# Optimization experiments

Hardware: AMD Instinct MI355X
Metric: run time of the kernel (lower is better)

The kernel has to match this reference:

```python
import jax, jax.numpy as jnp
import numpy as np

N = 20000       # num_nodes
B = 4           # batch
D = 32          # input_dim
OUT = 64        # output_dim
S = 2           # n_supports
E = 640000      # edges per support (avg degree 32)
MAX_STEP = 3
M = MAX_STEP * S + 1  # num_metrics = 7


def setup_inputs() -> dict:
    key = jax.random.key(0)
    k = jax.random.split(key, 6)
    inputs = jax.random.normal(k[0], (B, N, D), dtype=jnp.float32)
    edge_src = jax.random.randint(k[1], (S, E), 0, N, dtype=jnp.int32)
    edge_dst = jax.random.randint(k[2], (S, E), 0, N, dtype=jnp.int32)
    # ~1/deg scaled values so the diffusion recurrence stays numerically tame
    edge_vals = jax.random.uniform(k[3], (S, E), dtype=jnp.float32) / 32.0
    W = jax.random.normal(k[4], (OUT, D * M), dtype=jnp.float32) * 0.05
    bias = jnp.zeros((OUT,), dtype=jnp.float32)
    return dict(inputs=inputs, edge_vals=edge_vals, W=W, bias=bias,
                edge_src=edge_src, edge_dst=edge_dst)


def _spmm(vals, src, dst, x):
    # y[i] = sum_{edges (i<-j)} vals * x[j]  == support.mm(x) for COO support
    return jax.ops.segment_sum(vals[:, None] * x[src], dst, num_segments=N)


def reference(inputs, edge_vals, W, bias, edge_src, edge_dst):
    b, n, d = inputs.shape
    # x0: [N, D*B], batch fastest (matches permute([1,2,0]).reshape(n,-1))
    x0 = jnp.transpose(inputs, (1, 2, 0)).reshape(n, -1)
    xs = [x0]
    for s in range(S):
        v, sr, ds = edge_vals[s], edge_src[s], edge_dst[s]
        x1 = _spmm(v, sr, ds, x0)
        xs.append(x1)
        for _ in range(2, MAX_STEP + 1):
            x2 = 2.0 * _spmm(v, sr, ds, x1) - x0
            xs.append(x2)
            # NOTE: faithful to source aliasing quirk — x0 is mutated here,
            # so the next support starts from the mutated x0.
            x1, x0 = x2, x1
    x = jnp.stack(xs, 0)                       # [M, N, D*B]
    x = x.reshape(-1, n, d, b)                 # [M, N, D, B]
    x = jnp.transpose(x, (3, 1, 2, 0))         # [B, N, D, M]
    x = x.reshape(b, n, -1)                    # [B, N, D*M], M fastest
    return x @ W.T + bias                      # [B, N, OUT]
```

## Files before the change

kernel.cpp:

```cpp
#include <hip/hip_runtime.h>

#define N_NODES 20000
#define BATCH   4
#define DIN     32
#define DOUT    64
#define MSTEPS  7
#define ROW     128
#define NROW    896
#define NROWU   448
#define PLN     656
#define NT      79
#define KB2     (2 * NT)
#define CHUNK   2048
#define SLOT    12288
#define WSLOT   3584
#define RGRID   (N_NODES / 4)
#define PGRID   625
#define TGRID   10000

typedef short  short8 __attribute__((ext_vector_type(8)));
typedef float  f32x4  __attribute__((ext_vector_type(4)));

__device__ __forceinline__ unsigned short f2bf(float f) {
    unsigned u = __float_as_uint(f);
    unsigned r = u + 0x7fff + ((u >> 16) & 1);
    return (unsigned short)(r >> 16);
}
__device__ __forceinline__ float bf_lo(unsigned p) { return __uint_as_float(p << 16); }
__device__ __forceinline__ float bf_hi(unsigned p) { return __uint_as_float(p & 0xffff0000u); }

__global__ void init_k(int* __restrict__ cursor) {
    if (threadIdx.x < KB2) cursor[threadIdx.x] = threadIdx.x * SLOT;
}

__global__ void __launch_bounds__(256) p2t_k(const int* __restrict__ src,
                                             const int* __restrict__ dst,
                                             const float* __restrict__ vals,
                                             int* __restrict__ cursor,
                                             uint2* __restrict__ staged,
                                             const float* __restrict__ in,
                                             unsigned short* __restrict__ xs, int E) {
    __shared__ int lhist[KB2];
    __shared__ int lbase[KB2];
    __shared__ int gbase[KB2];
    __shared__ int sc[256];
    __shared__ uint2 buf[CHUNK];
    __shared__ unsigned short kk[CHUNK];
    int t = threadIdx.x;
    if (blockIdx.x >= PGRID) {
        int tid = (blockIdx.x - PGRID) * 256 + t;
        if (tid < N_NODES * ROW) {
            int b = tid & 3;
            int d = (tid >> 2) & 31;
            int n = tid >> 7;
            xs[(size_t)n * NROW + d * 4 + b] = f2bf(in[(b * N_NODES + n) * DIN + d]);
        }
        return;
    }
    int base = blockIdx.x * CHUNK;
    int nval = min(CHUNK, 2 * E - base);
    for (int i = t; i < KB2; i += 256) lhist[i] = 0;
    __syncthreads();
    int k[CHUNK / 256], pos[CHUNK / 256];
    uint2 pay[CHUNK / 256];
#pragma unroll
    for (int j = 0; j < CHUNK / 256; ++j) {
        int i = j * 256 + t;
        int e = base + i;
        if (i < nval) {
            int s = (e >= E) ? 1 : 0;
            int d = dst[e];
            pay[j] = make_uint2((unsigned)src[e] | ((unsigned)f2bf(vals[e]) << 16),
                                (unsigned)d);
            k[j] = s * NT + (d >> 8);
            pos[j] = atomicAdd(&lhist[k[j]], 1);
        } else k[j] = -1;
    }
    __syncthreads();
    int v = (t < KB2) ? lhist[t] : 0;
    sc[t] = v;
    __syncthreads();
    for (int off = 1; off < 256; off <<= 1) {
        int a = (t >= off) ? sc[t - off] : 0;
        __syncthreads();
        sc[t] += a;
        __syncthreads();
    }
    if (t < KB2) lbase[t] = sc[t] - v;
    __syncthreads();
    if (t < KB2 && lhist[t]) gbase[t] = atomicAdd(&cursor[t], lhist[t]);
#pragma unroll
    for (int j = 0; j < CHUNK / 256; ++j) {
        if (k[j] >= 0) {
            int slot = lbase[k[j]] + pos[j];
            buf[slot] = pay[j];
            kk[slot] = (unsigned short)k[j];
        }
    }
    __syncthreads();
#pragma unroll
    for (int j = 0; j < CHUNK / 256; ++j) {
        int i = j * 256 + t;
        if (i < nval) {
            int b = kk[i];
            staged[gbase[b] + (i - lbase[b])] = buf[i];
        }
    }
}

__global__ void __launch_bounds__(256) p3_fine_k(const uint2* __restrict__ staged,
                                                 const int* __restrict__ cursor,
                                                 int2* __restrict__ row_desc,
                                                 unsigned* __restrict__ csr) {
    __shared__ int lhist[64];
    __shared__ int sc[64];
    __shared__ int lcur[64];
    int bb = blockIdx.x;
    int b = bb >> 2, sub = bb & 3;
    int s = b / NT, tile = b - s * NT;
    int w0loc = sub * 64;
    int seg0 = b * SLOT;
    int len = cursor[b] - seg0;
    int t = threadIdx.x;
    if (t < 64) lhist[t] = 0;
    __syncthreads();
    for (int i = t; i < len; i += 256) {
        int dl = (int)(staged[seg0 + i].y & 255) - w0loc;
        if (dl >= 0 && dl < 64) atomicAdd(&lhist[dl], 1);
    }
    __syncthreads();
    int cntr = (t < 64) ? lhist[t] : 0;
    int pl = (cntr + 7) & ~7;
    if (t < 64) sc[t] = pl;
    __syncthreads();
    for (int off = 1; off < 64; off <<= 1) {
        int a = (t < 64 && t >= off) ? sc[t - off] : 0;
        __syncthreads();
        if (t < 64) sc[t] += a;
        __syncthreads();
    }
    int wbase = bb * WSLOT;
    if (t < 64) {
        int excl = sc[t] - pl;
        lcur[t] = wbase + excl;
        int nd = tile * 256 + w0loc + t;
        if (nd < N_NODES) row_desc[s * N_NODES + nd] = make_int2(wbase + excl, pl);
    }
    __syncthreads();
    for (int i = t; i < len; i += 256) {
        uint2 u = staged[seg0 + i];
        int dl = (int)(u.y & 255) - w0loc;
        if (dl >= 0 && dl < 64) {
            int p = atomicAdd(&lcur[dl], 1);
            csr[p] = u.x;
        }
    }
    if (t < 64) {
        int excl = sc[t] - pl;
        for (int i = cntr; i < pl; ++i) csr[wbase + excl + i] = 0u;
    }
}

__device__ __forceinline__ void spmm_core(const int2* __restrict__ rdesc,
                                          const unsigned* __restrict__ csr,
                                          const unsigned* __restrict__ xb,
                                          const unsigned* __restrict__ xprevb,
                                          unsigned* __restrict__ yb,
                                          float alpha, int node, int lane) {
    int2 rd = rdesc[node];
    int start = rd.x, end = rd.x + rd.y;
    float l0 = 0.f, h0 = 0.f, l1 = 0.f, h1 = 0.f;
    float l2 = 0.f, h2 = 0.f, l3 = 0.f, h3 = 0.f;
    for (int e = start; e < end; e += 8) {
        unsigned c0 = csr[e],     c1 = csr[e + 1], c2 = csr[e + 2], c3 = csr[e + 3];
        unsigned c4 = csr[e + 4], c5 = csr[e + 5], c6 = csr[e + 6], c7 = csr[e + 7];
        unsigned p0 = xb[(size_t)(c0 & 0xffffu) * NROWU + lane];
        unsigned p1 = xb[(size_t)(c1 & 0xffffu) * NROWU + lane];
        unsigned p2 = xb[(size_t)(c2 & 0xffffu) * NROWU + lane];
        unsigned p3 = xb[(size_t)(c3 & 0xffffu) * NROWU + lane];
        unsigned p4 = xb[(size_t)(c4 & 0xffffu) * NROWU + lane];
        unsigned p5 = xb[(size_t)(c5 & 0xffffu) * NROWU + lane];
        unsigned p6 = xb[(size_t)(c6 & 0xffffu) * NROWU + lane];
        unsigned p7 = xb[(size_t)(c7 & 0xffffu) * NROWU + lane];
        float v0 = bf_hi(c0), v1 = bf_hi(c1), v2 = bf_hi(c2), v3 = bf_hi(c3);
        float v4 = bf_hi(c4), v5 = bf_hi(c5), v6 = bf_hi(c6), v7 = bf_hi(c7);
        l0 = fmaf(v0, bf_lo(p0), l0);  h0 = fmaf(v0, bf_hi(p0), h0);
        l1 = fmaf(v1, bf_lo(p1), l1);  h1 = fmaf(v1, bf_hi(p1), h1);
        l2 = fmaf(v2, bf_lo(p2), l2);  h2 = fmaf(v2, bf_hi(p2), h2);
        l3 = fmaf(v3, bf_lo(p3), l3);  h3 = fmaf(v3, bf_hi(p3), h3);
        l0 = fmaf(v4, bf_lo(p4), l0);  h0 = fmaf(v4, bf_hi(p4), h0);
        l1 = fmaf(v5, bf_lo(p5), l1);  h1 = fmaf(v5, bf_hi(p5), h1);
        l2 = fmaf(v6, bf_lo(p6), l2);  h2 = fmaf(v6, bf_hi(p6), h2);
        l3 = fmaf(v7, bf_lo(p7), l3);  h3 = fmaf(v7, bf_hi(p7), h3);
    }
    float r0 = alpha * ((l0 + l1) + (l2 + l3));
    float r1 = alpha * ((h0 + h1) + (h2 + h3));
    if (xprevb) {
        unsigned pp = xprevb[(size_t)node * NROWU + lane];
        r0 -= bf_lo(pp);
        r1 -= bf_hi(pp);
    }
    yb[(size_t)node * NROWU + lane] = (unsigned)f2bf(r0) | ((unsigned)f2bf(r1) << 16);
}

__global__ void __launch_bounds__(256) spmm_row_k(const int2* __restrict__ rdesc,
                                                  const unsigned* __restrict__ csr,
                                                  const unsigned short* __restrict__ x,
                                                  const unsigned short* __restrict__ xprev,
                                                  unsigned short* __restrict__ y, float alpha) {
    int node = __builtin_amdgcn_readfirstlane(blockIdx.x * 4 + (threadIdx.x >> 6));
    int lane = threadIdx.x & 63;
    spmm_core(rdesc, csr, (const unsigned*)x, (const unsigned*)xprev, (unsigned*)y,
              alpha, node, lane);
}

__global__ void __launch_bounds__(256) spmm_dual_k(const int2* __restrict__ rdA,
                                                   const int2* __restrict__ rdB,
                                                   const unsigned* __restrict__ csr,
                                                   const unsigned short* __restrict__ x,
                                                   const unsigned short* __restrict__ xprevA,
                                                   unsigned short* __restrict__ yA,
                                                   unsigned short* __restrict__ yB) {
    int bid = blockIdx.x;
    int second = (bid >= RGRID) ? 1 : 0;
    int node = __builtin_amdgcn_readfirstlane((bid - second * RGRID) * 4 + (threadIdx.x >> 6));
    int lane = threadIdx.x & 63;
    const int2* rd = second ? rdB : rdA;
    const unsigned* xprevb = second ? nullptr : (const unsigned*)xprevA;
    unsigned* yb = second ? (unsigned*)yB : (unsigned*)yA;
    float alpha = second ? 1.0f : 2.0f;
    spmm_core(rd, csr, (const unsigned*)x, xprevb, yb, alpha, node, lane);
}

__global__ void __launch_bounds__(256) epilogue_mfma_k(const unsigned short* __restrict__ xs,
                                                       const float* __restrict__ W,
                                                       const float* __restrict__ bias,
                                                       float* __restrict__ out) {
    __shared__ unsigned short Alds[28 * PLN];
    int tid = threadIdx.x;
    int lane = tid & 63, ot = tid >> 6;
    int col = lane & 15, quad = lane >> 4;
    int o = ot * 16 + col;

    short8 bfrag[MSTEPS];
#pragma unroll
    for (int m = 0; m < MSTEPS; ++m) {
        short8 bf;
#pragma unroll
        for (int j = 0; j < 8; ++j)
            bf[j] = (short)f2bf(W[o * 224 + (quad * 8 + j) * 7 + m]);
        bfrag[m] = bf;
    }
    float bo = bias[o];

    int n0 = blockIdx.x * 16;
    const uint4* src = (const uint4*)(xs + (size_t)n0 * NROW);
#pragma unroll
    for (int it = 0; it < 7; ++it) {
        int idx = tid + it * 256;
        uint4 q = src[idx];
        int r    = idx / 112;
        int off8 = idx - r * 112;
        int m    = off8 >> 4;
        int d0   = (off8 & 15) * 2;
        unsigned vals[4] = {q.x, q.y, q.z, q.w};
#pragma unroll
        for (int h = 0; h < 4; ++h) {
            int dd = d0 + (h >> 1);
            int bA = (2 * h) & 3, bB = (2 * h + 1) & 3;
            Alds[(bA * 7 + m) * PLN + r * 40 + dd] = (unsigned short)(vals[h] & 0xffffu);
            Alds[(bB * 7 + m) * PLN + r * 40 + dd] = (unsigned short)(vals[h] >> 16);
        }
    }
    __syncthreads();

    f32x4 acc[BATCH];
#pragma unroll
    for (int b = 0; b < BATCH; ++b)
        acc[b] = (f32x4){bo, bo, bo, bo};

#pragma unroll
    for (int m = 0; m < MSTEPS; ++m) {
#pragma unroll
        for (int b = 0; b < BATCH; ++b) {
            short8 a = *(const short8*)&Alds[(b * 7 + m) * PLN + col * 40 + quad * 8];
            acc[b] = __builtin_amdgcn_mfma_f32_16x16x32_bf16(a, bfrag[m], acc[b], 0, 0, 0);
        }
    }

#pragma unroll
    for (int b = 0; b < BATCH; ++b) {
#pragma unroll
        for (int reg = 0; reg < 4; ++reg) {
            int n = n0 + quad * 4 + reg;
            out[((size_t)b * N_NODES + n) * DOUT + o] = acc[b][reg];
        }
    }
}

extern "C" void kernel_launch(void* const* d_in, const int* in_sizes, int n_in,
                              void* d_out, int out_size, void* d_ws, size_t ws_size,
                              hipStream_t stream) {
    const float* inputs    = (const float*)d_in[0];
    const float* edge_vals = (const float*)d_in[1];
    const float* W         = (const float*)d_in[2];
    const float* bias      = (const float*)d_in[3];
    const int*   edge_src  = (const int*)d_in[4];
    const int*   edge_dst  = (const int*)d_in[5];
    float* out = (float*)d_out;
    const int E = in_sizes[1] / 2;

    unsigned short* xs = (unsigned short*)d_ws;
    uint2* staged  = (uint2*)(xs + (size_t)N_NODES * NROW);
    unsigned* csr  = (unsigned*)(staged + (size_t)KB2 * SLOT);
    int* cursor    = (int*)(csr + (size_t)4 * KB2 * WSLOT);
    int2* row_desc = (int2*)(cursor + KB2 + 2);

    const int epgrid = N_NODES / 16;

    init_k<<<1, 256, 0, stream>>>(cursor);
    p2t_k<<<PGRID + TGRID, 256, 0, stream>>>(edge_src, edge_dst, edge_vals, cursor,
                                             staged, inputs, xs, E);
    p3_fine_k<<<4 * KB2, 256, 0, stream>>>(staged, cursor, row_desc, csr);

    const int2* rd0 = row_desc;
    const int2* rd1 = row_desc + N_NODES;

    unsigned short* X0 = xs + 0 * ROW;
    unsigned short* X1 = xs + 1 * ROW;
    unsigned short* X2 = xs + 2 * ROW;
    unsigned short* X3 = xs + 3 * ROW;
    unsigned short* X4 = xs + 4 * ROW;
    unsigned short* X5 = xs + 5 * ROW;
    unsigned short* X6 = xs + 6 * ROW;

    spmm_row_k<<<RGRID, 256, 0, stream>>>(rd0, csr, X0, nullptr, X1, 1.0f);
    spmm_row_k<<<RGRID, 256, 0, stream>>>(rd0, csr, X1, X0,      X2, 2.0f);
    spmm_dual_k<<<2 * RGRID, 256, 0, stream>>>(rd0, rd1, csr, X2, X1, X3, X4);
    spmm_row_k<<<RGRID, 256, 0, stream>>>(rd1, csr, X4, X2, X5, 2.0f);
    spmm_row_k<<<RGRID, 256, 0, stream>>>(rd1, csr, X5, X4, X6, 2.0f);

    epilogue_mfma_k<<<epgrid, 256, 0, stream>>>(xs, W, bias, out);
}
```

Baseline: 235.9 us.

## Fuse SpMM diffusion chain into one persistent kernel with grid barriers

Replaces the five separate SpMM launches with a single persistent kernel of 1024 blocks. Waves loop over nodes, and the dependent steps are separated by software grid-wide barriers built from an atomic counter. The aim is to remove launch gaps and per-launch ramp-up and tail costs between the dependent diffusion steps. In exchange it relies on all 1024 blocks being co-resident, since otherwise the barrier deadlocks. It also adds spin-wait cost and gives up the oversubscribed grid that helped hide latency.

```diff
diff --git a/kernel.cpp b/kernel.cpp
--- a/kernel.cpp
+++ b/kernel.cpp
@@ -14,9 +14,10 @@
 #define CHUNK   2048
 #define SLOT    12288
 #define WSLOT   3584
-#define RGRID   (N_NODES / 4)
 #define PGRID   625
 #define TGRID   10000
+#define CGRID   1024
+#define CWAVES  (CGRID * 4)
 
 typedef short  short8 __attribute__((ext_vector_type(8)));
 typedef float  f32x4  __attribute__((ext_vector_type(4)));
@@ -31,6 +32,7 @@
 
 __global__ void init_k(int* __restrict__ cursor) {
     if (threadIdx.x < KB2) cursor[threadIdx.x] = threadIdx.x * SLOT;
+    if (threadIdx.x == KB2) cursor[KB2] = 0;
 }
 
 __global__ void __launch_bounds__(256) p2t_k(const int* __restrict__ src,
@@ -203,33 +205,58 @@
     yb[(size_t)node * NROWU + lane] = (unsigned)f2bf(r0) | ((unsigned)f2bf(r1) << 16);
 }
 
-__global__ void __launch_bounds__(256) spmm_row_k(const int2* __restrict__ rdesc,
-                                                  const unsigned* __restrict__ csr,
-                                                  const unsigned short* __restrict__ x,
-                                                  const unsigned short* __restrict__ xprev,
-                                                  unsigned short* __restrict__ y, float alpha) {
-    int node = __builtin_amdgcn_readfirstlane(blockIdx.x * 4 + (threadIdx.x >> 6));
+__device__ __forceinline__ void gbar(int* bar, int phase) {
+    __syncthreads();
+    if (threadIdx.x == 0) {
+        __threadfence();
+        __hip_atomic_fetch_add(bar, 1, __ATOMIC_ACQ_REL, __HIP_MEMORY_SCOPE_AGENT);
+        int target = phase * CGRID;
+        while (__hip_atomic_load(bar, __ATOMIC_ACQUIRE, __HIP_MEMORY_SCOPE_AGENT) < target)
+            __builtin_amdgcn_s_sleep(2);
+        __threadfence();
+    }
+    __syncthreads();
+}
+
+__global__ void __launch_bounds__(256, 4) spmm_chain_k(const int2* __restrict__ rd0,
+                                                       const int2* __restrict__ rd1,
+                                                       const unsigned* __restrict__ csr,
+                                                       unsigned short* __restrict__ xs,
+                                                       int* __restrict__ bar) {
+    int wid = blockIdx.x * 4 + (threadIdx.x >> 6);
     int lane = threadIdx.x & 63;
-    spmm_core(rdesc, csr, (const unsigned*)x, (const unsigned*)xprev, (unsigned*)y,
-              alpha, node, lane);
-}
-
-__global__ void __launch_bounds__(256) spmm_dual_k(const int2* __restrict__ rdA,
-                                                   const int2* __restrict__ rdB,
-                                                   const unsigned* __restrict__ csr,
-                                                   const unsigned short* __restrict__ x,
-                                                   const unsigned short* __restrict__ xprevA,
-                                                   unsigned short* __restrict__ yA,
-                                                   unsigned short* __restrict__ yB) {
-    int bid = blockIdx.x;
-    int second = (bid >= RGRID) ? 1 : 0;
-    int node = __builtin_amdgcn_readfirstlane((bid - second * RGRID) * 4 + (threadIdx.x >> 6));
-    int lane = threadIdx.x & 63;
-    const int2* rd = second ? rdB : rdA;
-    const unsigned* xprevb = second ? nullptr : (const unsigned*)xprevA;
-    unsigned* yb = second ? (unsigned*)yB : (unsigned*)yA;
-    float alpha = second ? 1.0f : 2.0f;
-    spmm_core(rd, csr, (const unsigned*)x, xprevb, yb, alpha, node, lane);
+    unsigned* X0 = (unsigned*)xs + 0 * 64;
+    unsigned* X1 = (unsigned*)xs + 1 * 64;
+    unsigned* X2 = (unsigned*)xs + 2 * 64;
+    unsigned* X3 = (unsigned*)xs + 3 * 64;
+    unsigned* X4 = (unsigned*)xs + 4 * 64;
+    unsigned* X5 = (unsigned*)xs + 5 * 64;
+    unsigned* X6 = (unsigned*)xs + 6 * 64;
+
+    for (int n = wid; n < N_NODES; n += CWAVES)
+        spmm_core(rd0, csr, X0, nullptr, X1, 1.0f,
+                  __builtin_amdgcn_readfirstlane(n), lane);
+    gbar(bar, 1);
+    for (int n = wid; n < N_NODES; n += CWAVES)
+        spmm_core(rd0, csr, X1, X0, X2, 2.0f,
+                  __builtin_amdgcn_readfirstlane(n), lane);
+    gbar(bar, 2);
+    for (int t = wid; t < 2 * N_NODES; t += CWAVES) {
+        if (t < N_NODES)
+            spmm_core(rd0, csr, X2, X1, X3, 2.0f,
+                      __builtin_amdgcn_readfirstlane(t), lane);
+        else
+            spmm_core(rd1, csr, X2, nullptr, X4, 1.0f,
+                      __builtin_amdgcn_readfirstlane(t - N_NODES), lane);
+    }
+    gbar(bar, 3);
+    for (int n = wid; n < N_NODES; n += CWAVES)
+        spmm_core(rd1, csr, X4, X2, X5, 2.0f,
+                  __builtin_amdgcn_readfirstlane(n), lane);
+    gbar(bar, 4);
+    for (int n = wid; n < N_NODES; n += CWAVES)
+        spmm_core(rd1, csr, X5, X4, X6, 2.0f,
+                  __builtin_amdgcn_readfirstlane(n), lane);
 }
 
 __global__ void __launch_bounds__(256) epilogue_mfma_k(const unsigned short* __restrict__ xs,
@@ -315,6 +342,7 @@
     unsigned* csr  = (unsigned*)(staged + (size_t)KB2 * SLOT);
     int* cursor    = (int*)(csr + (size_t)4 * KB2 * WSLOT);
     int2* row_desc = (int2*)(cursor + KB2 + 2);
+    int* bar       = cursor + KB2;
 
     const int epgrid = N_NODES / 16;
 
@@ -326,19 +354,7 @@
     const int2* rd0 = row_desc;
     const int2* rd1 = row_desc + N_NODES;
 
-    unsigned short* X0 = xs + 0 * ROW;
-    unsigned short* X1 = xs + 1 * ROW;
-    unsigned short* X2 = xs + 2 * ROW;
-    unsigned short* X3 = xs + 3 * ROW;
-    unsigned short* X4 = xs + 4 * ROW;
-    unsigned short* X5 = xs + 5 * ROW;
-    unsigned short* X6 = xs + 6 * ROW;
-
-    spmm_row_k<<<RGRID, 256, 0, stream>>>(rd0, csr, X0, nullptr, X1, 1.0f);
-    spmm_row_k<<<RGRID, 256, 0, stream>>>(rd0, csr, X1, X0,      X2, 2.0f);
-    spmm_dual_k<<<2 * RGRID, 256, 0, stream>>>(rd0, rd1, csr, X2, X1, X3, X4);
-    spmm_row_k<<<RGRID, 256, 0, stream>>>(rd1, csr, X4, X2, X5, 2.0f);
-    spmm_row_k<<<RGRID, 256, 0, stream>>>(rd1, csr, X5, X4, X6, 2.0f);
+    spmm_chain_k<<<CGRID, 256, 0, stream>>>(rd0, rd1, csr, xs, bar);
 
     epilogue_mfma_k<<<epgrid, 256, 0, stream>>>(xs, W, bias, out);
 }
```

New measurement: 903.4 us. 283% more time.

## Build CSR via global histogram, scan, and atomic scatter instead of bucket staging

Applied to the files above, without the earlier changes.

Replaces the two-pass bucketed staging CSR build with a classic counting-sort pipeline: zero a per-row histogram, count degrees with global atomics, block-scan padded degrees, add block offsets and zero-pad, then scatter each edge directly into its CSR slot through per-row atomic cursors. This drops the intermediate staged buffer and its second read pass. In exchange it adds extra kernel launches and relies on global atomics with poor scatter locality. Row order within the CSR also becomes nondeterministic.

```diff
diff --git a/kernel.cpp b/kernel.cpp
--- a/kernel.cpp
+++ b/kernel.cpp
@@ -9,13 +9,9 @@
 #define NROW    896
 #define NROWU   448
 #define PLN     656
-#define NT      79
-#define KB2     (2 * NT)
-#define CHUNK   2048
-#define SLOT    12288
-#define WSLOT   3584
+#define NROWS2  (2 * N_NODES)
+#define SBLK    157
 #define RGRID   (N_NODES / 4)
-#define PGRID   625
 #define TGRID   10000
 
 typedef short  short8 __attribute__((ext_vector_type(8)));
@@ -29,56 +25,29 @@
 __device__ __forceinline__ float bf_lo(unsigned p) { return __uint_as_float(p << 16); }
 __device__ __forceinline__ float bf_hi(unsigned p) { return __uint_as_float(p & 0xffff0000u); }
 
-__global__ void init_k(int* __restrict__ cursor) {
-    if (threadIdx.x < KB2) cursor[threadIdx.x] = threadIdx.x * SLOT;
-}
-
-__global__ void __launch_bounds__(256) p2t_k(const int* __restrict__ src,
-                                             const int* __restrict__ dst,
-                                             const float* __restrict__ vals,
-                                             int* __restrict__ cursor,
-                                             uint2* __restrict__ staged,
-                                             const float* __restrict__ in,
-                                             unsigned short* __restrict__ xs, int E) {
-    __shared__ int lhist[KB2];
-    __shared__ int lbase[KB2];
-    __shared__ int gbase[KB2];
+__global__ void __launch_bounds__(256) zero_k(int* __restrict__ hist) {
+    int i = blockIdx.x * 256 + threadIdx.x;
+    if (i < NROWS2) hist[i] = 0;
+}
+
+__global__ void __launch_bounds__(256) hist_k(const int* __restrict__ dst,
+                                              int* __restrict__ hist, int E) {
+    int e = blockIdx.x * 256 + threadIdx.x;
+    if (e < 2 * E) {
+        int s = (e >= E) ? N_NODES : 0;
+        atomicAdd(&hist[s + dst[e]], 1);
+    }
+}
+
+__global__ void __launch_bounds__(256) scan1_k(const int* __restrict__ hist,
+                                               int2* __restrict__ row_desc,
+                                               int* __restrict__ bsum) {
     __shared__ int sc[256];
-    __shared__ uint2 buf[CHUNK];
-    __shared__ unsigned short kk[CHUNK];
     int t = threadIdx.x;
-    if (blockIdx.x >= PGRID) {
-        int tid = (blockIdx.x - PGRID) * 256 + t;
-        if (tid < N_NODES * ROW) {
-            int b = tid & 3;
-            int d = (tid >> 2) & 31;
-            int n = tid >> 7;
-            xs[(size_t)n * NROW + d * 4 + b] = f2bf(in[(b * N_NODES + n) * DIN + d]);
-        }
-        return;
-    }
-    int base = blockIdx.x * CHUNK;
-    int nval = min(CHUNK, 2 * E - base);
-    for (int i = t; i < KB2; i += 256) lhist[i] = 0;
-    __syncthreads();
-    int k[CHUNK / 256], pos[CHUNK / 256];
-    uint2 pay[CHUNK / 256];
-#pragma unroll
-    for (int j = 0; j < CHUNK / 256; ++j) {
-        int i = j * 256 + t;
-        int e = base + i;
-        if (i < nval) {
-            int s = (e >= E) ? 1 : 0;
-            int d = dst[e];
-            pay[j] = make_uint2((unsigned)src[e] | ((unsigned)f2bf(vals[e]) << 16),
-                                (unsigned)d);
-            k[j] = s * NT + (d >> 8);
-            pos[j] = atomicAdd(&lhist[k[j]], 1);
-        } else k[j] = -1;
-    }
-    __syncthreads();
-    int v = (t < KB2) ? lhist[t] : 0;
-    sc[t] = v;
+    int i = blockIdx.x * 256 + t;
+    int deg = (i < NROWS2) ? hist[i] : 0;
+    int pl = (deg + 7) & ~7;
+    sc[t] = pl;
     __syncthreads();
     for (int off = 1; off < 256; off <<= 1) {
         int a = (t >= off) ? sc[t - off] : 0;
@@ -86,78 +55,59 @@
         sc[t] += a;
         __syncthreads();
     }
-    if (t < KB2) lbase[t] = sc[t] - v;
+    if (i < NROWS2) row_desc[i] = make_int2(sc[t] - pl, pl);
+    if (t == 255) bsum[blockIdx.x] = sc[t];
+}
+
+__global__ void __launch_bounds__(256) fin_k(int2* __restrict__ row_desc,
+                                             const int* __restrict__ bsum,
+                                             const int* __restrict__ hist,
+                                             int* __restrict__ cursor,
+                                             unsigned* __restrict__ csr) {
+    __shared__ int red[256];
+    int t = threadIdx.x;
+    int blk = blockIdx.x;
+    red[t] = (t < blk) ? bsum[t] : 0;
     __syncthreads();
-    if (t < KB2 && lhist[t]) gbase[t] = atomicAdd(&cursor[t], lhist[t]);
-#pragma unroll
-    for (int j = 0; j < CHUNK / 256; ++j) {
-        if (k[j] >= 0) {
-            int slot = lbase[k[j]] + pos[j];
-            buf[slot] = pay[j];
-            kk[slot] = (unsigned short)k[j];
-        }
-    }
-    __syncthreads();
-#pragma unroll
-    for (int j = 0; j < CHUNK / 256; ++j) {
-        int i = j * 256 + t;
-        if (i < nval) {
-            int b = kk[i];
-            staged[gbase[b] + (i - lbase[b])] = buf[i];
-        }
-    }
-}
-
-__global__ void __launch_bounds__(256) p3_fine_k(const uint2* __restrict__ staged,
-                                                 const int* __restrict__ cursor,
-                                                 int2* __restrict__ row_desc,
-                                                 unsigned* __restrict__ csr) {
-    __shared__ int lhist[64];
-    __shared__ int sc[64];
-    __shared__ int lcur[64];
-    int bb = blockIdx.x;
-    int b = bb >> 2, sub = bb & 3;
-    int s = b / NT, tile = b - s * NT;
-    int w0loc = sub * 64;
-    int seg0 = b * SLOT;
-    int len = cursor[b] - seg0;
+    for (int off = 128; off > 0; off >>= 1) {
+        if (t < off) red[t] += red[t + off];
+        __syncthreads();
+    }
+    int boff = red[0];
+    int i = blk * 256 + t;
+    if (i >= NROWS2) return;
+    int2 rdv = row_desc[i];
+    int start = rdv.x + boff;
+    int deg = hist[i];
+    row_desc[i] = make_int2(start, rdv.y);
+    cursor[i] = start;
+    for (int j = deg; j < rdv.y; ++j) csr[start + j] = 0u;
+}
+
+__global__ void __launch_bounds__(256) scat_k(const int* __restrict__ src,
+                                              const int* __restrict__ dst,
+                                              const float* __restrict__ vals,
+                                              int* __restrict__ cursor,
+                                              unsigned* __restrict__ csr,
+                                              const float* __restrict__ in,
+                                              unsigned short* __restrict__ xs,
+                                              int E, int sgrid) {
     int t = threadIdx.x;
-    if (t < 64) lhist[t] = 0;
-    __syncthreads();
-    for (int i = t; i < len; i += 256) {
-        int dl = (int)(staged[seg0 + i].y & 255) - w0loc;
-        if (dl >= 0 && dl < 64) atomicAdd(&lhist[dl], 1);
-    }
-    __syncthreads();
-    int cntr = (t < 64) ? lhist[t] : 0;
-    int pl = (cntr + 7) & ~7;
-    if (t < 64) sc[t] = pl;
-    __syncthreads();
-    for (int off = 1; off < 64; off <<= 1) {
-        int a = (t < 64 && t >= off) ? sc[t - off] : 0;
-        __syncthreads();
-        if (t < 64) sc[t] += a;
-        __syncthreads();
-    }
-    int wbase = bb * WSLOT;
-    if (t < 64) {
-        int excl = sc[t] - pl;
-        lcur[t] = wbase + excl;
-        int nd = tile * 256 + w0loc + t;
-        if (nd < N_NODES) row_desc[s * N_NODES + nd] = make_int2(wbase + excl, pl);
-    }
-    __syncthreads();
-    for (int i = t; i < len; i += 256) {
-        uint2 u = staged[seg0 + i];
-        int dl = (int)(u.y & 255) - w0loc;
-        if (dl >= 0 && dl < 64) {
-            int p = atomicAdd(&lcur[dl], 1);
-            csr[p] = u.x;
-        }
-    }
-    if (t < 64) {
-        int excl = sc[t] - pl;
-        for (int i = cntr; i < pl; ++i) csr[wbase + excl + i] = 0u;
+    if (blockIdx.x >= sgrid) {
+        int tid = (blockIdx.x - sgrid) * 256 + t;
+        if (tid < N_NODES * ROW) {
+            int b = tid & 3;
+            int d = (tid >> 2) & 31;
+            int n = tid >> 7;
+            xs[(size_t)n * NROW + d * 4 + b] = f2bf(in[(b * N_NODES + n) * DIN + d]);
+        }
+        return;
+    }
+    int e = blockIdx.x * 256 + t;
+    if (e < 2 * E) {
+        int s = (e >= E) ? N_NODES : 0;
+        int pos = atomicAdd(&cursor[s + dst[e]], 1);
+        csr[pos] = (unsigned)src[e] | ((unsigned)f2bf(vals[e]) << 16);
     }
 }
 
@@ -311,17 +261,21 @@
     const int E = in_sizes[1] / 2;
 
     unsigned short* xs = (unsigned short*)d_ws;
-    uint2* staged  = (uint2*)(xs + (size_t)N_NODES * NROW);
-    unsigned* csr  = (unsigned*)(staged + (size_t)KB2 * SLOT);
-    int* cursor    = (int*)(csr + (size_t)4 * KB2 * WSLOT);
-    int2* row_desc = (int2*)(cursor + KB2 + 2);
+    unsigned* csr  = (unsigned*)(xs + (size_t)N_NODES * NROW);
+    int* hist      = (int*)(csr + ((size_t)2 * E + 8 * NROWS2));
+    int* cursor    = hist + NROWS2;
+    int2* row_desc = (int2*)(cursor + NROWS2);
+    int* bsum      = (int*)(row_desc + NROWS2);
 
     const int epgrid = N_NODES / 16;
-
-    init_k<<<1, 256, 0, stream>>>(cursor);
-    p2t_k<<<PGRID + TGRID, 256, 0, stream>>>(edge_src, edge_dst, edge_vals, cursor,
-                                             staged, inputs, xs, E);
-    p3_fine_k<<<4 * KB2, 256, 0, stream>>>(staged, cursor, row_desc, csr);
+    const int egrid  = (2 * E + 255) / 256;
+
+    zero_k<<<SBLK, 256, 0, stream>>>(hist);
+    hist_k<<<egrid, 256, 0, stream>>>(edge_dst, hist, E);
+    scan1_k<<<SBLK, 256, 0, stream>>>(hist, row_desc, bsum);
+    fin_k<<<SBLK, 256, 0, stream>>>(row_desc, bsum, hist, cursor, csr);
+    scat_k<<<egrid + TGRID, 256, 0, stream>>>(edge_src, edge_dst, edge_vals,
+                                              cursor, csr, inputs, xs, E, egrid);
 
     const int2* rd0 = row_desc;
     const int2* rd1 = row_desc + N_NODES;
```

Result: slower. 342.2 us (+45.1%).
